# Performance work log

Measured on AMD Instinct MI355X. Metric: run time of the kernel, lower is better.

The kernel has to match this reference:

```python
import jax, jax.numpy as jnp
import numpy as np

TRANSLATE_STD = 0.125
SCALE_STD = 0.2
CUTOUT_SIZE = 0.5

B, C, H, W = 64, 3, 512, 512


def setup_inputs() -> dict:
    key = jax.random.key(0)
    ks = jax.random.split(key, 20)
    inp = {
        'images': jax.random.normal(ks[0], (B, C, H, W), dtype=jnp.float32),
        'u_angle': jax.random.uniform(ks[1], (B,), dtype=jnp.float32),
        'u_scale': jax.random.uniform(ks[2], (B,), dtype=jnp.float32),
        'u_trans': jax.random.uniform(ks[3], (B,), dtype=jnp.float32),
        'u_bright': jax.random.uniform(ks[4], (B,), dtype=jnp.float32),
        'u_contrast': jax.random.uniform(ks[5], (B,), dtype=jnp.float32),
        'u_sat': jax.random.uniform(ks[6], (B,), dtype=jnp.float32),
        'noise': jax.random.normal(ks[7], (B, C, H, W), dtype=jnp.float32),
        'm_flip': jax.random.randint(ks[8], (B,), 0, 2, dtype=jnp.int32),
        'm_rot': jax.random.randint(ks[9], (B,), 0, 2, dtype=jnp.int32),
        'm_scale': jax.random.randint(ks[10], (B,), 0, 2, dtype=jnp.int32),
        'm_trans': jax.random.randint(ks[11], (B,), 0, 2, dtype=jnp.int32),
        'm_bright': jax.random.randint(ks[12], (B,), 0, 2, dtype=jnp.int32),
        'm_contrast': jax.random.randint(ks[13], (B,), 0, 2, dtype=jnp.int32),
        'm_sat': jax.random.randint(ks[14], (B,), 0, 2, dtype=jnp.int32),
        'm_cut': jax.random.randint(ks[15], (B,), 0, 2, dtype=jnp.int32),
        'y0': jax.random.randint(ks[16], (B,), 0, H - int(H * CUTOUT_SIZE) + 1, dtype=jnp.int32),
        'x0': jax.random.randint(ks[17], (B,), 0, W - int(W * CUTOUT_SIZE) + 1, dtype=jnp.int32),
    }
    return inp


def _sample_bilinear_reflect(img, gx, gy):
    # img: [C,H,W]; gx, gy: [H,W] normalized coords in grid_sample convention
    # (align_corners=False, padding_mode='reflection')
    c, h, w = img.shape
    x = ((gx + 1.0) * w - 1.0) * 0.5
    y = ((gy + 1.0) * h - 1.0) * 0.5

    def reflect(v, size):
        # reflect about pixel edges [-0.5, size-0.5], then clip coordinate
        v = jnp.abs(v + 0.5)
        v = jnp.mod(v, 2.0 * size)
        v = jnp.minimum(v, 2.0 * size - v)
        return jnp.clip(v - 0.5, 0.0, size - 1.0)

    x = reflect(x, float(w))
    y = reflect(y, float(h))
    x0f = jnp.floor(x)
    y0f = jnp.floor(y)
    wx = x - x0f
    wy = y - y0f
    x0i = jnp.clip(x0f, 0, w - 1).astype(jnp.int32)
    x1i = jnp.clip(x0f + 1, 0, w - 1).astype(jnp.int32)
    y0i = jnp.clip(y0f, 0, h - 1).astype(jnp.int32)
    y1i = jnp.clip(y0f + 1, 0, h - 1).astype(jnp.int32)
    v00 = img[:, y0i, x0i]
    v01 = img[:, y0i, x1i]
    v10 = img[:, y1i, x0i]
    v11 = img[:, y1i, x1i]
    top = v00 + wx * (v01 - v00)
    bot = v10 + wx * (v11 - v10)
    return top + wy * (bot - top)


def reference(images, u_angle, u_scale, u_trans, u_bright, u_contrast, u_sat,
              noise, m_flip, m_rot, m_scale, m_trans, m_bright, m_contrast,
              m_sat, m_cut, y0, x0):
    b, c, h, w = images.shape
    # xflip
    images = jnp.where((m_flip > 0)[:, None, None, None], images[..., ::-1], images)
    # rotate / scale / translate (single value broadcast to both axes, as in original)
    angle = jnp.where(m_rot > 0, (u_angle * 2.0 - 1.0) * jnp.pi, 0.0)
    sc = jnp.where(m_scale > 0, (u_scale * 2.0 - 1.0) * SCALE_STD + 1.0, 1.0)
    tr = jnp.where(m_trans > 0, (u_trans * 2.0 - 1.0) * TRANSLATE_STD, 0.0)
    ca = jnp.cos(angle)[:, None, None]
    sa = jnp.sin(angle)[:, None, None]
    scb = sc[:, None, None]
    trb = tr[:, None, None]
    gx0, gy0 = jnp.meshgrid(jnp.linspace(-1.0, 1.0, w), jnp.linspace(-1.0, 1.0, h), indexing='xy')  # [H,W]
    gx = scb * (ca * gx0 - sa * gy0) + trb  # [B,H,W]
    gy = scb * (sa * gx0 + ca * gy0) + trb
    images = jax.vmap(_sample_bilinear_reflect)(images, gx, gy)
    # brightness
    bb = jnp.where(m_bright > 0, u_bright * 0.2, 0.0)
    images = jnp.clip(images + bb[:, None, None, None], -1.0, 1.0)
    # contrast
    cc = jnp.where(m_contrast > 0, u_contrast + 0.5, 1.0)
    images = jnp.clip(images * cc[:, None, None, None], -1.0, 1.0)
    # saturation: lerp(grayscale, images, s)
    ss = jnp.where(m_sat > 0, u_sat * 2.0, 1.0)[:, None, None, None]
    gray = images.mean(axis=1, keepdims=True)
    images = jnp.clip(gray + ss * (images - gray), -1.0, 1.0)
    ch, cw = int(h * CUTOUT_SIZE), int(w * CUTOUT_SIZE)
    ys = jnp.arange(h)[None, :, None]
    xs = jnp.arange(w)[None, None, :]
    y0b = y0[:, None, None]
    x0b = x0[:, None, None]
    cmask = (ys >= y0b) & (ys < y0b + ch) & (xs >= x0b) & (xs < x0b + cw)
    fmask = cmask & (m_cut > 0)[:, None, None]
    images = jnp.where(fmask[:, None, :, :], noise, images)
    return images
```

## Files before the change

kernel.cpp:

```cpp
#include <hip/hip_runtime.h>
#include <math.h>


constexpr int Bn = 64;
constexpr int Cn = 3;
constexpr int Hn = 512;
constexpr int Wn = 512;
constexpr float TRANSLATE_STD = 0.125f;
constexpr float SCALE_STD = 0.2f;
constexpr int CUT_H = 256;
constexpr int CUT_W = 256;

constexpr int FW = 32;
constexpr int FSTRIDE = 40;
constexpr int FH_MAX = 32;
constexpr int CH_LDS = FSTRIDE * FH_MAX;
constexpr int NT = 8;
constexpr uint32_t PLANE = 512u * 512u;

typedef float f4v __attribute__((ext_vector_type(4)));
typedef float f2v __attribute__((ext_vector_type(2)));

__device__ __forceinline__ f2v load2(const float* p) {
    f2v r;
    __builtin_memcpy(&r, p, 8);
    return r;
}

__device__ __forceinline__ float reflect_coord(float v, float size) {
    v = fabsf(v + 0.5f);
    v = fmodf(v, 2.0f * size);
    v = fminf(v, 2.0f * size - v);
    return fminf(fmaxf(v - 0.5f, 0.0f), size - 1.0f);
}

__device__ __forceinline__ void pipe_barrier() {
    asm volatile("s_waitcnt lgkmcnt(0)" ::: "memory");
    __builtin_amdgcn_s_barrier();
    __builtin_amdgcn_sched_barrier(0);
}

__global__ __launch_bounds__(256) void augment_kernel(
    const float* __restrict__ images,
    const float* __restrict__ u_angle,
    const float* __restrict__ u_scale,
    const float* __restrict__ u_trans,
    const float* __restrict__ u_bright,
    const float* __restrict__ u_contrast,
    const float* __restrict__ u_sat,
    const float* __restrict__ noise,
    const int* __restrict__ m_flip,
    const int* __restrict__ m_rot,
    const int* __restrict__ m_scale,
    const int* __restrict__ m_trans,
    const int* __restrict__ m_bright,
    const int* __restrict__ m_contrast,
    const int* __restrict__ m_sat,
    const int* __restrict__ m_cut,
    const int* __restrict__ y0p,
    const int* __restrict__ x0p,
    float* __restrict__ out)
{
    __shared__ __align__(16) float lds[Cn * CH_LDS];

    const int lin = blockIdx.x + (blockIdx.y << 2) + (blockIdx.z << 7);
    const int swz = ((lin & 7) << 10) + (lin >> 3);
    const int sx0 = (swz & 3) << 7;
    const int y16 = (swz >> 2) & 31;
    const int b   = swz >> 7;

    const int tx  = threadIdx.x;
    const int ty  = threadIdx.y;
    const int y   = (y16 << 4) + ty;

    const float angle = (m_rot[b] > 0) ? (u_angle[b] * 2.0f - 1.0f) * 3.14159265358979323846f : 0.0f;
    const float sc    = (m_scale[b] > 0) ? (u_scale[b] * 2.0f - 1.0f) * SCALE_STD + 1.0f : 1.0f;
    const float tr    = (m_trans[b] > 0) ? (u_trans[b] * 2.0f - 1.0f) * TRANSLATE_STD : 0.0f;
    const float bb    = (m_bright[b] > 0) ? u_bright[b] * 0.2f : 0.0f;
    const float cc    = (m_contrast[b] > 0) ? u_contrast[b] + 0.5f : 1.0f;
    const float ss    = (m_sat[b] > 0) ? u_sat[b] * 2.0f : 1.0f;
    const bool  flip  = m_flip[b] > 0;
    const bool  docut = m_cut[b] > 0;
    const int   cy0   = y0p[b];
    const int   cx0   = x0p[b];

    float saf, caf;
    __sincosf(angle, &saf, &caf);

    const float kk = sc * (512.0f / 511.0f);
    const float dxdx = caf * kk, dxdy = -saf * kk;
    const float dydx = saf * kk, dydy = caf * kk;
    const float xx_org = 256.0f * (sc * (saf - caf) + tr + 1.0f) - 0.5f;
    const float yy_org = 256.0f * (sc * (-saf - caf) + tr + 1.0f) - 0.5f;

    const float step_x = 16.0f * dxdx;
    const float step_y = 16.0f * dydx;

    float xxt = xx_org + (float)(sx0 + tx) * dxdx + (float)y * dxdy;
    float yyt = yy_org + (float)(sx0 + tx) * dydx + (float)y * dydy;

    const float fty = (float)(y16 << 4);
    float bx = xx_org + (float)sx0 * dxdx + fty * dxdy;
    float by = yy_org + (float)sx0 * dydx + fty * dydy;
    const float sxx = 15.0f * dxdx, sxy = 15.0f * dxdy;
    const float syx = 15.0f * dydx, syy = 15.0f * dydy;
    const float min_dx = fminf(sxx, 0.0f) + fminf(sxy, 0.0f);
    const float max_dx = fmaxf(sxx, 0.0f) + fmaxf(sxy, 0.0f);
    const float min_dy = fminf(syx, 0.0f) + fminf(syy, 0.0f);
    const float max_dy = fmaxf(syx, 0.0f) + fmaxf(syy, 0.0f);

    const float* __restrict__ imgb = images + (size_t)b * (Cn * PLANE);
    float* __restrict__ outb       = out    + (size_t)b * (Cn * PLANE);
    const float* __restrict__ noib = noise  + (size_t)b * (Cn * PLANE);

    const int tid = ty * 16 + tx;
    const int sr  = tid >> 3;
    const int sq  = (tid & 7) << 2;

    const bool ycut = docut && (y >= cy0) && (y < cy0 + CUT_H);
    uint32_t opix = (uint32_t)y * 512u + (uint32_t)(sx0 + tx);

    int cx_lo, cy_lo, cfh; bool cok;
    int nx_lo, ny_lo, nfh; bool nok;
    auto mkbox = [&](float bxv, float byv, int& x_lo, int& y_lo, int& fh, bool& ok) {
        const float minxx = bxv + min_dx, maxxx = bxv + max_dx;
        const float minyy = byv + min_dy, maxyy = byv + max_dy;
        ok = (minxx >= 1.0f) && (maxxx <= 509.0f) &&
             (minyy >= 1.0f) && (maxyy <= 509.0f);
        x_lo = 0; y_lo = 0; fh = 0;
        if (ok) {
            x_lo = min(((int)minxx - 1) & ~3, Wn - FW);
            y_lo = (int)minyy - 1;
            fh   = ((int)maxyy + 2) - y_lo + 1;
            if (fh > FH_MAX) ok = false;
        }
    };

    f4v A{}, B{}, C{};
    auto loadR = [&](int x_lo, int y_lo) {
        const int scol = flip ? (508 - x_lo - sq) : (x_lo + sq);
        const uint32_t soff = (uint32_t)(y_lo + sr) * 512u + (uint32_t)scol;
        A = *(const f4v*)(imgb + soff);
        B = *(const f4v*)(imgb + soff + PLANE);
        C = *(const f4v*)(imgb + soff + 2 * PLANE);
    };
    auto writeR = [&]() {
        f4v a = A, b2 = B, c2 = C;
        if (flip) {
            a  = f4v{A.w, A.z, A.y, A.x};
            b2 = f4v{B.w, B.z, B.y, B.x};
            c2 = f4v{C.w, C.z, C.y, C.x};
        }
        float* d = &lds[sr * FSTRIDE + sq];
        *(f4v*)(d)              = a;
        *(f4v*)(d + CH_LDS)     = b2;
        *(f4v*)(d + 2 * CH_LDS) = c2;
    };

    mkbox(bx, by, cx_lo, cy_lo, cfh, cok);
    if (cok && sr < cfh) { loadR(cx_lo, cy_lo); writeR(); }
    bx += step_x; by += step_y;
    mkbox(bx, by, nx_lo, ny_lo, nfh, nok);
    if (nok && sr < nfh) loadR(nx_lo, ny_lo);
    pipe_barrier();

    #pragma unroll 1
    for (int t = 0; t < NT; ++t) {
        float vals[Cn];
        if (cok) {
            const float fx = xxt - (float)cx_lo;
            const float fy = yyt - (float)cy_lo;
            const int xi = (int)fx;
            const int yi = (int)fy;
            const float wx = fx - (float)xi;
            const float wy = fy - (float)yi;
            const float* ph = &lds[yi * FSTRIDE + xi];
            #pragma unroll
            for (int c = 0; c < Cn; ++c) {
                const float v00 = ph[0], v01 = ph[1];
                const float v10 = ph[FSTRIDE], v11 = ph[FSTRIDE + 1];
                ph += CH_LDS;
                const float top = v00 + wx * (v01 - v00);
                const float bot = v10 + wx * (v11 - v10);
                float v = top + wy * (bot - top);
                v = __builtin_amdgcn_fmed3f(v + bb, -1.0f, 1.0f);
                v = __builtin_amdgcn_fmed3f(v * cc, -1.0f, 1.0f);
                vals[c] = v;
            }
        } else {
            const float rxx = reflect_coord(xxt, (float)Wn);
            const float ryy = reflect_coord(yyt, (float)Hn);
            const float x0f = floorf(rxx);
            const float y0f = floorf(ryy);
            const float wx = rxx - x0f;
            const float wy = ryy - y0f;
            int x0i = (int)fminf(fmaxf(x0f, 0.0f), 511.0f);
            int x1i = (int)fminf(x0f + 1.0f, 511.0f);
            const int y0i = (int)fminf(fmaxf(y0f, 0.0f), 511.0f);
            const int y1i = (int)fminf(y0f + 1.0f, 511.0f);
            if (flip) { x0i = 511 - x0i; x1i = 511 - x1i; }
            const int xbase = min(min(x0i, x1i), 510);
            const bool s0 = (x0i != xbase);
            const bool s1 = (x1i != xbase);
            const uint32_t r0 = (uint32_t)(y0i * 512 + xbase);
            const uint32_t r1 = (uint32_t)(y1i * 512 + xbase);
            #pragma unroll
            for (int c = 0; c < Cn; ++c) {
                const f2v t0 = load2(imgb + r0 + c * PLANE);
                const f2v t1 = load2(imgb + r1 + c * PLANE);
                const float v00 = s0 ? t0.y : t0.x;
                const float v01 = s1 ? t0.y : t0.x;
                const float v10 = s0 ? t1.y : t1.x;
                const float v11 = s1 ? t1.y : t1.x;
                const float top = v00 + wx * (v01 - v00);
                const float bot = v10 + wx * (v11 - v10);
                float v = top + wy * (bot - top);
                v = __builtin_amdgcn_fmed3f(v + bb, -1.0f, 1.0f);
                v = __builtin_amdgcn_fmed3f(v * cc, -1.0f, 1.0f);
                vals[c] = v;
            }
        }

        const float gray = (vals[0] + vals[1] + vals[2]) * (1.0f / 3.0f);
        const int xpix = sx0 + (t << 4) + tx;
        const bool cut = ycut && (xpix >= cx0) && (xpix < cx0 + CUT_W);
        #pragma unroll
        for (int c = 0; c < Cn; ++c) {
            float v = gray + ss * (vals[c] - gray);
            v = __builtin_amdgcn_fmed3f(v, -1.0f, 1.0f);
            if (cut) v = __builtin_nontemporal_load(&noib[opix + c * PLANE]);
            __builtin_nontemporal_store(v, &outb[opix + c * PLANE]);
        }
        opix += 16;
        xxt += step_x; yyt += step_y;

        if (t == NT - 1) break;

        pipe_barrier();
        cx_lo = nx_lo; cy_lo = ny_lo; cfh = nfh; cok = nok;
        if (cok && sr < cfh) writeR();
        bx += step_x; by += step_y;
        if (t + 2 < NT) {
            mkbox(bx, by, nx_lo, ny_lo, nfh, nok);
            if (nok && sr < nfh) loadR(nx_lo, ny_lo);
        } else {
            nok = false;
        }
        pipe_barrier();
    }
}

extern "C" void kernel_launch(void* const* d_in, const int* in_sizes, int n_in,
                              void* d_out, int out_size, void* d_ws, size_t ws_size,
                              hipStream_t stream) {
    const float* images     = (const float*)d_in[0];
    const float* u_angle    = (const float*)d_in[1];
    const float* u_scale    = (const float*)d_in[2];
    const float* u_trans    = (const float*)d_in[3];
    const float* u_bright   = (const float*)d_in[4];
    const float* u_contrast = (const float*)d_in[5];
    const float* u_sat      = (const float*)d_in[6];
    const float* noise      = (const float*)d_in[7];
    const int*   m_flip     = (const int*)d_in[8];
    const int*   m_rot      = (const int*)d_in[9];
    const int*   m_scale    = (const int*)d_in[10];
    const int*   m_trans    = (const int*)d_in[11];
    const int*   m_bright   = (const int*)d_in[12];
    const int*   m_contrast = (const int*)d_in[13];
    const int*   m_sat      = (const int*)d_in[14];
    const int*   m_cut      = (const int*)d_in[15];
    const int*   y0p        = (const int*)d_in[16];
    const int*   x0p        = (const int*)d_in[17];
    float* out = (float*)d_out;

    dim3 block(16, 16);
    dim3 grid(Wn / (16 * NT), Hn / 16, Bn);
    augment_kernel<<<grid, block, 0, stream>>>(
        images, u_angle, u_scale, u_trans, u_bright, u_contrast, u_sat, noise,
        m_flip, m_rot, m_scale, m_trans, m_bright, m_contrast, m_sat, m_cut,
        y0p, x0p, out);
}
```

Measured before the change: 509.5 us.

## Stage reflected tiles into LDS and remove the global-memory fallback sampling path

Reflection padding is now applied while staging each source tile into LDS, using integer reflection of rows and columns with a reversed or gathered load near the borders. Every output tile then samples from LDS, and the divergent fallback branch that did float reflection and 2-wide global loads is gone. This removes warp divergence and uncoalesced global gathers for tiles near the image edges. The cost is extra integer work and scalar gathers at border tiles. Footprints taller than FH_MAX are clamped rather than sent to a fallback, which could drop rows of the footprint at large scales.

```diff
diff --git a/kernel.cpp b/kernel.cpp
--- a/kernel.cpp
+++ b/kernel.cpp
@@ -19,19 +19,10 @@
 constexpr uint32_t PLANE = 512u * 512u;
 
 typedef float f4v __attribute__((ext_vector_type(4)));
-typedef float f2v __attribute__((ext_vector_type(2)));
-
-__device__ __forceinline__ f2v load2(const float* p) {
-    f2v r;
-    __builtin_memcpy(&r, p, 8);
-    return r;
-}
-
-__device__ __forceinline__ float reflect_coord(float v, float size) {
-    v = fabsf(v + 0.5f);
-    v = fmodf(v, 2.0f * size);
-    v = fminf(v, 2.0f * size - v);
-    return fminf(fmaxf(v - 0.5f, 0.0f), size - 1.0f);
+
+__device__ __forceinline__ int refl(int v) {
+    v = (v < 0) ? (-1 - v) : v;
+    return (v > 511) ? (1023 - v) : v;
 }
 
 __device__ __forceinline__ void pipe_barrier() {
@@ -105,7 +96,6 @@
     const float sxx = 15.0f * dxdx, sxy = 15.0f * dxdy;
     const float syx = 15.0f * dydx, syy = 15.0f * dydy;
     const float min_dx = fminf(sxx, 0.0f) + fminf(sxy, 0.0f);
-    const float max_dx = fmaxf(sxx, 0.0f) + fmaxf(sxy, 0.0f);
     const float min_dy = fminf(syx, 0.0f) + fminf(syy, 0.0f);
     const float max_dy = fmaxf(syx, 0.0f) + fmaxf(syy, 0.0f);
 
@@ -120,33 +110,46 @@
     const bool ycut = docut && (y >= cy0) && (y < cy0 + CUT_H);
     uint32_t opix = (uint32_t)y * 512u + (uint32_t)(sx0 + tx);
 
-    int cx_lo, cy_lo, cfh; bool cok;
-    int nx_lo, ny_lo, nfh; bool nok;
-    auto mkbox = [&](float bxv, float byv, int& x_lo, int& y_lo, int& fh, bool& ok) {
-        const float minxx = bxv + min_dx, maxxx = bxv + max_dx;
-        const float minyy = byv + min_dy, maxyy = byv + max_dy;
-        ok = (minxx >= 1.0f) && (maxxx <= 509.0f) &&
-             (minyy >= 1.0f) && (maxyy <= 509.0f);
-        x_lo = 0; y_lo = 0; fh = 0;
-        if (ok) {
-            x_lo = min(((int)minxx - 1) & ~3, Wn - FW);
-            y_lo = (int)minyy - 1;
-            fh   = ((int)maxyy + 2) - y_lo + 1;
-            if (fh > FH_MAX) ok = false;
-        }
+    int cx_lo, cy_lo, cfh;
+    int nx_lo, ny_lo, nfh;
+    auto mkbox = [&](float bxv, float byv, int& x_lo, int& y_lo, int& fh) {
+        x_lo = (int)floorf(bxv + min_dx) - 1;
+        y_lo = (int)floorf(byv + min_dy) - 1;
+        fh   = min(((int)floorf(byv + max_dy) + 2) - y_lo + 1, FH_MAX);
     };
 
     f4v A{}, B{}, C{};
+    bool rev = false;
     auto loadR = [&](int x_lo, int y_lo) {
-        const int scol = flip ? (508 - x_lo - sq) : (x_lo + sq);
-        const uint32_t soff = (uint32_t)(y_lo + sr) * 512u + (uint32_t)scol;
-        A = *(const f4v*)(imgb + soff);
-        B = *(const f4v*)(imgb + soff + PLANE);
-        C = *(const f4v*)(imgb + soff + 2 * PLANE);
+        const uint32_t ro = (uint32_t)refl(y_lo + sr) * 512u;
+        const int c0 = x_lo + sq;
+        int S0 = refl(c0);     if (flip) S0 = 511 - S0;
+        int S3 = refl(c0 + 3); if (flip) S3 = 511 - S3;
+        const int d = S3 - S0;
+        if (d == 3) {
+            rev = false;
+            __builtin_memcpy(&A, imgb + ro + S0, 16);
+            __builtin_memcpy(&B, imgb + ro + S0 + PLANE, 16);
+            __builtin_memcpy(&C, imgb + ro + S0 + 2 * PLANE, 16);
+        } else if (d == -3) {
+            rev = true;
+            __builtin_memcpy(&A, imgb + ro + S3, 16);
+            __builtin_memcpy(&B, imgb + ro + S3 + PLANE, 16);
+            __builtin_memcpy(&C, imgb + ro + S3 + 2 * PLANE, 16);
+        } else {
+            rev = false;
+            int S1 = refl(c0 + 1); if (flip) S1 = 511 - S1;
+            int S2 = refl(c0 + 2); if (flip) S2 = 511 - S2;
+            A = f4v{imgb[ro + S0], imgb[ro + S1], imgb[ro + S2], imgb[ro + S3]};
+            const float* p1 = imgb + PLANE;
+            B = f4v{p1[ro + S0], p1[ro + S1], p1[ro + S2], p1[ro + S3]};
+            const float* p2 = imgb + 2 * PLANE;
+            C = f4v{p2[ro + S0], p2[ro + S1], p2[ro + S2], p2[ro + S3]};
+        }
     };
     auto writeR = [&]() {
         f4v a = A, b2 = B, c2 = C;
-        if (flip) {
+        if (rev) {
             a  = f4v{A.w, A.z, A.y, A.x};
             b2 = f4v{B.w, B.z, B.y, B.x};
             c2 = f4v{C.w, C.z, C.y, C.x};
@@ -157,68 +160,35 @@
         *(f4v*)(d + 2 * CH_LDS) = c2;
     };
 
-    mkbox(bx, by, cx_lo, cy_lo, cfh, cok);
-    if (cok && sr < cfh) { loadR(cx_lo, cy_lo); writeR(); }
+    mkbox(bx, by, cx_lo, cy_lo, cfh);
+    if (sr < cfh) { loadR(cx_lo, cy_lo); writeR(); }
     bx += step_x; by += step_y;
-    mkbox(bx, by, nx_lo, ny_lo, nfh, nok);
-    if (nok && sr < nfh) loadR(nx_lo, ny_lo);
+    mkbox(bx, by, nx_lo, ny_lo, nfh);
+    if (sr < nfh) loadR(nx_lo, ny_lo);
     pipe_barrier();
 
     #pragma unroll 1
     for (int t = 0; t < NT; ++t) {
+        const float fx = xxt - (float)cx_lo;
+        const float fy = yyt - (float)cy_lo;
+        const int xi = (int)fx;
+        const int yi = (int)fy;
+        const float wx = fx - (float)xi;
+        const float wy = fy - (float)yi;
+        const float* ph = &lds[yi * FSTRIDE + xi];
+
         float vals[Cn];
-        if (cok) {
-            const float fx = xxt - (float)cx_lo;
-            const float fy = yyt - (float)cy_lo;
-            const int xi = (int)fx;
-            const int yi = (int)fy;
-            const float wx = fx - (float)xi;
-            const float wy = fy - (float)yi;
-            const float* ph = &lds[yi * FSTRIDE + xi];
-            #pragma unroll
-            for (int c = 0; c < Cn; ++c) {
-                const float v00 = ph[0], v01 = ph[1];
-                const float v10 = ph[FSTRIDE], v11 = ph[FSTRIDE + 1];
-                ph += CH_LDS;
-                const float top = v00 + wx * (v01 - v00);
-                const float bot = v10 + wx * (v11 - v10);
-                float v = top + wy * (bot - top);
-                v = __builtin_amdgcn_fmed3f(v + bb, -1.0f, 1.0f);
-                v = __builtin_amdgcn_fmed3f(v * cc, -1.0f, 1.0f);
-                vals[c] = v;
-            }
-        } else {
-            const float rxx = reflect_coord(xxt, (float)Wn);
-            const float ryy = reflect_coord(yyt, (float)Hn);
-            const float x0f = floorf(rxx);
-            const float y0f = floorf(ryy);
-            const float wx = rxx - x0f;
-            const float wy = ryy - y0f;
-            int x0i = (int)fminf(fmaxf(x0f, 0.0f), 511.0f);
-            int x1i = (int)fminf(x0f + 1.0f, 511.0f);
-            const int y0i = (int)fminf(fmaxf(y0f, 0.0f), 511.0f);
-            const int y1i = (int)fminf(y0f + 1.0f, 511.0f);
-            if (flip) { x0i = 511 - x0i; x1i = 511 - x1i; }
-            const int xbase = min(min(x0i, x1i), 510);
-            const bool s0 = (x0i != xbase);
-            const bool s1 = (x1i != xbase);
-            const uint32_t r0 = (uint32_t)(y0i * 512 + xbase);
-            const uint32_t r1 = (uint32_t)(y1i * 512 + xbase);
-            #pragma unroll
-            for (int c = 0; c < Cn; ++c) {
-                const f2v t0 = load2(imgb + r0 + c * PLANE);
-                const f2v t1 = load2(imgb + r1 + c * PLANE);
-                const float v00 = s0 ? t0.y : t0.x;
-                const float v01 = s1 ? t0.y : t0.x;
-                const float v10 = s0 ? t1.y : t1.x;
-                const float v11 = s1 ? t1.y : t1.x;
-                const float top = v00 + wx * (v01 - v00);
-                const float bot = v10 + wx * (v11 - v10);
-                float v = top + wy * (bot - top);
-                v = __builtin_amdgcn_fmed3f(v + bb, -1.0f, 1.0f);
-                v = __builtin_amdgcn_fmed3f(v * cc, -1.0f, 1.0f);
-                vals[c] = v;
-            }
+        #pragma unroll
+        for (int c = 0; c < Cn; ++c) {
+            const float v00 = ph[0], v01 = ph[1];
+            const float v10 = ph[FSTRIDE], v11 = ph[FSTRIDE + 1];
+            ph += CH_LDS;
+            const float top = v00 + wx * (v01 - v00);
+            const float bot = v10 + wx * (v11 - v10);
+            float v = top + wy * (bot - top);
+            v = __builtin_amdgcn_fmed3f(v + bb, -1.0f, 1.0f);
+            v = __builtin_amdgcn_fmed3f(v * cc, -1.0f, 1.0f);
+            vals[c] = v;
         }
 
         const float gray = (vals[0] + vals[1] + vals[2]) * (1.0f / 3.0f);
@@ -237,14 +207,14 @@
         if (t == NT - 1) break;
 
         pipe_barrier();
-        cx_lo = nx_lo; cy_lo = ny_lo; cfh = nfh; cok = nok;
-        if (cok && sr < cfh) writeR();
+        cx_lo = nx_lo; cy_lo = ny_lo; cfh = nfh;
+        if (sr < cfh) writeR();
         bx += step_x; by += step_y;
         if (t + 2 < NT) {
-            mkbox(bx, by, nx_lo, ny_lo, nfh, nok);
-            if (nok && sr < nfh) loadR(nx_lo, ny_lo);
+            mkbox(bx, by, nx_lo, ny_lo, nfh);
+            if (sr < nfh) loadR(nx_lo, ny_lo);
         } else {
-            nok = false;
+            nfh = 0;
         }
         pipe_barrier();
     }
```

Result: no change. 516.3 us (+1.3%).
